# Optimization experiments

Hardware: AMD Instinct MI355X
Metric: run time of the kernel (lower is better)

Reference implementation:

```python
import jax, jax.numpy as jnp
import numpy as np


def setup_inputs() -> dict:
    key = jax.random.key(0)
    k1, k2, k3 = jax.random.split(key, 3)
    Na, Nb, K, D = 1024, 1024, 256, 128
    a = jax.random.normal(k1, (Na, D), dtype=jnp.float32)
    b = jax.random.normal(k2, (Nb, D), dtype=jnp.float32)
    feats = jax.random.normal(k3, (K, D), dtype=jnp.float32)
    return {"a": a, "b": b, "feats": feats}


def reference(a, b, feats):
    # mode='ignorematch'
    a_fk = a @ feats.T            # [Na, K]
    b_fk = b @ feats.T            # [Nb, K]
    a_e = a_fk[:, None, :]        # [Na, 1, K]
    b_e = b_fk[None, :, :]        # [1, Nb, K]
    mask = ((a_e > 0) & (b_e <= 0)).astype(a_fk.dtype)  # [Na, Nb, K]
    result = jnp.sum(a_e * mask, axis=2)                # [Na, Nb]
    return result
```

## Files before the change

kernel.cpp:

```cpp
#include <hip/hip_runtime.h>
#include <hip/hip_bf16.h>

typedef __attribute__((ext_vector_type(4))) float f32x4;
typedef __attribute__((ext_vector_type(2))) double f64x2;
typedef __attribute__((ext_vector_type(8))) short short8;

#define NA 1024
#define NB 1024
#define KF 256
#define DIM 128

#define RB 32
#define CB 64
#define FPAD 130

__global__ __launch_bounds__(256) void proj_kernel(
    const float* __restrict__ a, const float* __restrict__ b,
    const float* __restrict__ feats,
    __hip_bfloat16* __restrict__ P, __hip_bfloat16* __restrict__ M)
{
    __shared__ double Xd[RB][FPAD];
    __shared__ double Fd[CB][FPAD];

    const int t = threadIdx.x;
    const int rowBlk = blockIdx.x >> 2;
    const int colBlk = blockIdx.x & 3;
    const int row0 = rowBlk * RB;
    const int col0 = colBlk * CB;

    const bool isA = row0 < NA;
    const float* __restrict__ src = isA ? a : b;
    const int r0 = isA ? row0 : row0 - NA;

#pragma unroll
    for (int i = 0; i < 4; ++i) {
        int idx = t + i * 256;
        int r = idx >> 5, c4 = idx & 31;
        f32x4 v = ((const f32x4*)(src + (size_t)(r0 + r) * DIM))[c4];
#pragma unroll
        for (int j = 0; j < 4; ++j) Xd[r][c4 * 4 + j] = (double)v[j];
    }
#pragma unroll
    for (int i = 0; i < 8; ++i) {
        int idx = t + i * 256;
        int r = idx >> 5, c4 = idx & 31;
        f32x4 v = ((const f32x4*)(feats + (size_t)(col0 + r) * DIM))[c4];
#pragma unroll
        for (int j = 0; j < 4; ++j) Fd[r][c4 * 4 + j] = (double)v[j];
    }
    __syncthreads();

    const int rg = t >> 5;
    const int cl = t & 31;

    double acc[4][2] = {{0.0, 0.0}, {0.0, 0.0}, {0.0, 0.0}, {0.0, 0.0}};

#pragma unroll 2
    for (int d = 0; d < DIM; d += 4) {
        f64x2 xa[4][2], fa[2][2];
#pragma unroll
        for (int r = 0; r < 4; ++r) {
            xa[r][0] = *(const f64x2*)&Xd[rg * 4 + r][d];
            xa[r][1] = *(const f64x2*)&Xd[rg * 4 + r][d + 2];
        }
        fa[0][0] = *(const f64x2*)&Fd[cl][d];
        fa[0][1] = *(const f64x2*)&Fd[cl][d + 2];
        fa[1][0] = *(const f64x2*)&Fd[cl + 32][d];
        fa[1][1] = *(const f64x2*)&Fd[cl + 32][d + 2];
#pragma unroll
        for (int r = 0; r < 4; ++r)
#pragma unroll
            for (int h = 0; h < 2; ++h)
#pragma unroll
                for (int j = 0; j < 2; ++j) {
                    acc[r][0] = fma(xa[r][h][j], fa[0][h][j], acc[r][0]);
                    acc[r][1] = fma(xa[r][h][j], fa[1][h][j], acc[r][1]);
                }
    }

    if (isA) {
#pragma unroll
        for (int r = 0; r < 4; ++r) {
            size_t grow = (size_t)(r0 + rg * 4 + r) * KF;
            float v0 = (acc[r][0] > 0.0) ? (float)acc[r][0] : 0.0f;
            float v1 = (acc[r][1] > 0.0) ? (float)acc[r][1] : 0.0f;
            P[grow + col0 + cl] = __float2bfloat16(v0);
            P[grow + col0 + cl + 32] = __float2bfloat16(v1);
        }
    } else {
#pragma unroll
        for (int r = 0; r < 4; ++r) {
            size_t grow = (size_t)(r0 + rg * 4 + r) * KF;
            float v0 = (acc[r][0] <= 0.0) ? 1.0f : 0.0f;
            float v1 = (acc[r][1] <= 0.0) ? 1.0f : 0.0f;
            M[grow + col0 + cl] = __float2bfloat16(v0);
            M[grow + col0 + cl + 32] = __float2bfloat16(v1);
        }
    }
}

__global__ __launch_bounds__(256) void gemm_kernel(
    const __hip_bfloat16* __restrict__ P, const __hip_bfloat16* __restrict__ M,
    float* __restrict__ out)
{
    __shared__ short LA[64][264];
    __shared__ short LB[64][264];
    const int t = threadIdx.x;
    const int row0 = blockIdx.y * 64;
    const int col0 = blockIdx.x * 64;
    const short* Pa = (const short*)P;
    const short* Mb = (const short*)M;

#pragma unroll
    for (int i = 0; i < 8; ++i) {
        int c = t + i * 256;
        int row = c >> 5;
        int c8 = (c & 31) << 3;
        *(short8*)&LA[row][c8] = *(const short8*)(Pa + (size_t)(row0 + row) * KF + c8);
        *(short8*)&LB[row][c8] = *(const short8*)(Mb + (size_t)(col0 + row) * KF + c8);
    }
    __syncthreads();

    const int lane = t & 63;
    const int wid = t >> 6;
    const int wr = (wid >> 1) * 32;
    const int wc = (wid & 1) * 32;
    const int fr = lane & 15;
    const int fq = lane >> 4;

    f32x4 acc[2][2];
#pragma unroll
    for (int m = 0; m < 2; ++m)
#pragma unroll
        for (int n = 0; n < 2; ++n)
            acc[m][n] = (f32x4){0.f, 0.f, 0.f, 0.f};

#pragma unroll
    for (int kk = 0; kk < KF / 32; ++kk) {
        const int kb = kk * 32 + fq * 8;
        short8 a0 = *(const short8*)&LA[wr + fr][kb];
        short8 a1 = *(const short8*)&LA[wr + 16 + fr][kb];
        short8 b0 = *(const short8*)&LB[wc + fr][kb];
        short8 b1 = *(const short8*)&LB[wc + 16 + fr][kb];
        acc[0][0] = __builtin_amdgcn_mfma_f32_16x16x32_bf16(a0, b0, acc[0][0], 0, 0, 0);
        acc[0][1] = __builtin_amdgcn_mfma_f32_16x16x32_bf16(a0, b1, acc[0][1], 0, 0, 0);
        acc[1][0] = __builtin_amdgcn_mfma_f32_16x16x32_bf16(a1, b0, acc[1][0], 0, 0, 0);
        acc[1][1] = __builtin_amdgcn_mfma_f32_16x16x32_bf16(a1, b1, acc[1][1], 0, 0, 0);
    }

#pragma unroll
    for (int m = 0; m < 2; ++m)
#pragma unroll
        for (int n = 0; n < 2; ++n)
#pragma unroll
            for (int r = 0; r < 4; ++r) {
                int row = row0 + wr + m * 16 + fq * 4 + r;
                int col = col0 + wc + n * 16 + fr;
                out[(size_t)row * NB + col] = acc[m][n][r];
            }
}

extern "C" void kernel_launch(void* const* d_in, const int* in_sizes, int n_in,
                              void* d_out, int out_size, void* d_ws, size_t ws_size,
                              hipStream_t stream) {
    const float* a = (const float*)d_in[0];
    const float* b = (const float*)d_in[1];
    const float* feats = (const float*)d_in[2];
    float* out = (float*)d_out;
    __hip_bfloat16* P = (__hip_bfloat16*)d_ws;
    __hip_bfloat16* M = P + (size_t)NA * KF;

    proj_kernel<<<dim3(256), dim3(256), 0, stream>>>(a, b, feats, P, M);
    gemm_kernel<<<dim3(NB / 64, NA / 64), dim3(256), 0, stream>>>(P, M, out);
}
```

Baseline: 15.91 us.

## Load projection rows via wave-uniform scalar loads and widen feature tile

Restructures the fp64 projection kernel so each block covers 16 rows and 128 features. The input rows are no longer staged in LDS; each wave reads its 4 rows through wave-uniform (readfirstlane) addresses with a one-step register prefetch. Each lane handles two features 64 apart, and the grid changes from 256 to 256 blocks of a different shape, with feats staged twice as large per block. This removes the row LDS buffer and its broadcast reads, at the cost of more feats traffic per block and larger LDS use per block.

Measured after the change: 18.65 us. 1.17x slower.

```diff
diff --git a/kernel.cpp b/kernel.cpp
--- a/kernel.cpp
+++ b/kernel.cpp
@@ -10,91 +10,95 @@
 #define KF 256
 #define DIM 128
 
-#define RB 32
-#define CB 64
-#define FPAD 130
+#define RB 16
+#define CBLK 128
+#define FP 130
 
 __global__ __launch_bounds__(256) void proj_kernel(
     const float* __restrict__ a, const float* __restrict__ b,
     const float* __restrict__ feats,
     __hip_bfloat16* __restrict__ P, __hip_bfloat16* __restrict__ M)
 {
-    __shared__ double Xd[RB][FPAD];
-    __shared__ double Fd[CB][FPAD];
+    __shared__ double Fd[CBLK][FP];
 
     const int t = threadIdx.x;
-    const int rowBlk = blockIdx.x >> 2;
-    const int colBlk = blockIdx.x & 3;
+    const int rowBlk = blockIdx.x >> 1;
+    const int colBlk = blockIdx.x & 1;
     const int row0 = rowBlk * RB;
-    const int col0 = colBlk * CB;
+    const int col0 = colBlk * CBLK;
 
     const bool isA = row0 < NA;
     const float* __restrict__ src = isA ? a : b;
     const int r0 = isA ? row0 : row0 - NA;
 
 #pragma unroll
-    for (int i = 0; i < 4; ++i) {
+    for (int i = 0; i < 16; ++i) {
         int idx = t + i * 256;
-        int r = idx >> 5, c4 = idx & 31;
-        f32x4 v = ((const f32x4*)(src + (size_t)(r0 + r) * DIM))[c4];
-#pragma unroll
-        for (int j = 0; j < 4; ++j) Xd[r][c4 * 4 + j] = (double)v[j];
-    }
-#pragma unroll
-    for (int i = 0; i < 8; ++i) {
-        int idx = t + i * 256;
-        int r = idx >> 5, c4 = idx & 31;
-        f32x4 v = ((const f32x4*)(feats + (size_t)(col0 + r) * DIM))[c4];
-#pragma unroll
-        for (int j = 0; j < 4; ++j) Fd[r][c4 * 4 + j] = (double)v[j];
+        int c = idx >> 5, q = idx & 31;
+        f32x4 v = ((const f32x4*)(feats + (size_t)(col0 + c) * DIM))[q];
+        *(f64x2*)&Fd[c][q * 4] = (f64x2){(double)v[0], (double)v[1]};
+        *(f64x2*)&Fd[c][q * 4 + 2] = (f64x2){(double)v[2], (double)v[3]};
     }
     __syncthreads();
 
-    const int rg = t >> 5;
-    const int cl = t & 31;
+    const int wid = t >> 6;
+    const int l = t & 63;
+
+    const float* __restrict__ xp =
+        src + (size_t)__builtin_amdgcn_readfirstlane(r0 + wid * 4) * DIM;
 
     double acc[4][2] = {{0.0, 0.0}, {0.0, 0.0}, {0.0, 0.0}, {0.0, 0.0}};
 
+    f32x4 xc[4];
+#pragma unroll
+    for (int r = 0; r < 4; ++r) xc[r] = *(const f32x4*)(xp + r * DIM);
+
 #pragma unroll 2
     for (int d = 0; d < DIM; d += 4) {
-        f64x2 xa[4][2], fa[2][2];
+        f32x4 xn[4];
+        if (d + 4 < DIM) {
+#pragma unroll
+            for (int r = 0; r < 4; ++r) xn[r] = *(const f32x4*)(xp + r * DIM + d + 4);
+        }
+        f64x2 f0[2], f1[2];
+        f0[0] = *(const f64x2*)&Fd[l][d];
+        f0[1] = *(const f64x2*)&Fd[l][d + 2];
+        f1[0] = *(const f64x2*)&Fd[l + 64][d];
+        f1[1] = *(const f64x2*)&Fd[l + 64][d + 2];
 #pragma unroll
         for (int r = 0; r < 4; ++r) {
-            xa[r][0] = *(const f64x2*)&Xd[rg * 4 + r][d];
-            xa[r][1] = *(const f64x2*)&Xd[rg * 4 + r][d + 2];
+            double x0 = (double)xc[r][0], x1 = (double)xc[r][1];
+            double x2 = (double)xc[r][2], x3 = (double)xc[r][3];
+            acc[r][0] = fma(x0, f0[0][0], acc[r][0]);
+            acc[r][0] = fma(x1, f0[0][1], acc[r][0]);
+            acc[r][0] = fma(x2, f0[1][0], acc[r][0]);
+            acc[r][0] = fma(x3, f0[1][1], acc[r][0]);
+            acc[r][1] = fma(x0, f1[0][0], acc[r][1]);
+            acc[r][1] = fma(x1, f1[0][1], acc[r][1]);
+            acc[r][1] = fma(x2, f1[1][0], acc[r][1]);
+            acc[r][1] = fma(x3, f1[1][1], acc[r][1]);
         }
-        fa[0][0] = *(const f64x2*)&Fd[cl][d];
-        fa[0][1] = *(const f64x2*)&Fd[cl][d + 2];
-        fa[1][0] = *(const f64x2*)&Fd[cl + 32][d];
-        fa[1][1] = *(const f64x2*)&Fd[cl + 32][d + 2];
 #pragma unroll
-        for (int r = 0; r < 4; ++r)
-#pragma unroll
-            for (int h = 0; h < 2; ++h)
-#pragma unroll
-                for (int j = 0; j < 2; ++j) {
-                    acc[r][0] = fma(xa[r][h][j], fa[0][h][j], acc[r][0]);
-                    acc[r][1] = fma(xa[r][h][j], fa[1][h][j], acc[r][1]);
-                }
+        for (int r = 0; r < 4; ++r) xc[r] = xn[r];
     }
 
     if (isA) {
 #pragma unroll
         for (int r = 0; r < 4; ++r) {
-            size_t grow = (size_t)(r0 + rg * 4 + r) * KF;
+            size_t grow = (size_t)(r0 + wid * 4 + r) * KF;
             float v0 = (acc[r][0] > 0.0) ? (float)acc[r][0] : 0.0f;
             float v1 = (acc[r][1] > 0.0) ? (float)acc[r][1] : 0.0f;
-            P[grow + col0 + cl] = __float2bfloat16(v0);
-            P[grow + col0 + cl + 32] = __float2bfloat16(v1);
+            P[grow + col0 + l] = __float2bfloat16(v0);
+            P[grow + col0 + l + 64] = __float2bfloat16(v1);
         }
     } else {
 #pragma unroll
         for (int r = 0; r < 4; ++r) {
-            size_t grow = (size_t)(r0 + rg * 4 + r) * KF;
+            size_t grow = (size_t)(r0 + wid * 4 + r) * KF;
             float v0 = (acc[r][0] <= 0.0) ? 1.0f : 0.0f;
             float v1 = (acc[r][1] <= 0.0) ? 1.0f : 0.0f;
-            M[grow + col0 + cl] = __float2bfloat16(v0);
-            M[grow + col0 + cl + 32] = __float2bfloat16(v1);
+            M[grow + col0 + l] = __float2bfloat16(v0);
+            M[grow + col0 + l + 64] = __float2bfloat16(v1);
         }
     }
 }
```
